# Kernel tuning notes

Hardware: AMD Instinct MI355X
Metric: run time of the kernel (lower is better)

Reference implementation:

```python
import jax, jax.numpy as jnp
import numpy as np


def pw_dist_sq(X, Y):
    xx = jnp.sum(X * X, axis=1)[:, None]   # [N,1]
    yy = jnp.sum(Y * Y, axis=1)[None, :]   # [1,N]
    xy = X @ Y.T                            # [N,N]
    return jnp.maximum(xx + yy - 2.0 * xy, 0.0)


def setup_inputs() -> dict:
    key = jax.random.key(0)
    k1, k2 = jax.random.split(key)
    N, D = 1024, 128
    X = jax.random.normal(k1, (N, D), dtype=jnp.float32)
    Y = jax.random.normal(k2, (N, D), dtype=jnp.float32)
    return {"X": X, "Y": Y, "h": 1}


def reference(X, Y, h):
    h = float(h)
    inv_h2 = 1.0 / (h * h)
    sq_dists = pw_dist_sq(X, Y)                       # [N,N]
    K = jnp.exp(-0.5 * inv_h2 * sq_dists)             # [N,N]
    # d_K[i,j,:] = -(X[i]-Y[j])/h^2 * K[i,j]; returned reduced over j
    diff = X[:, None, :] - Y[None, :, :]              # [N,N,D]
    d_K_sum = jnp.sum(-diff * inv_h2 * K[:, :, None], axis=1)  # [N,D]
    return K, d_K_sum
```

## Files before the change

kernel.cpp:

```cpp
#include <hip/hip_runtime.h>

#define NN 1024
#define DD 128

typedef float f32x4 __attribute__((ext_vector_type(4)));
typedef _Float16 f16x4 __attribute__((ext_vector_type(4)));
typedef _Float16 f16x8 __attribute__((ext_vector_type(8)));

__device__ __forceinline__ f16x8 cvt8(f32x4 a, f32x4 b) {
  f16x8 r;
  r[0] = (_Float16)a.x; r[1] = (_Float16)a.y; r[2] = (_Float16)a.z; r[3] = (_Float16)a.w;
  r[4] = (_Float16)b.x; r[5] = (_Float16)b.y; r[6] = (_Float16)b.z; r[7] = (_Float16)b.w;
  return r;
}

__device__ __forceinline__ void bar_lds() {
  asm volatile("s_waitcnt lgkmcnt(0)" ::: "memory");
  __builtin_amdgcn_s_barrier();
  asm volatile("" ::: "memory");
}

#define WS_PART 8192

__global__ __launch_bounds__(256, 2) void gk_main(const float* __restrict__ X,
                                                  const float* __restrict__ Y,
                                                  const int* __restrict__ hp,
                                                  float* __restrict__ out,
                                                  float* __restrict__ ws) {
  __shared__ __align__(16) _Float16 Ks[16][136];
  __shared__ unsigned msc[16];
  __shared__ float Sred[16];

  const int tid  = threadIdx.x;
  const int js   = blockIdx.x;
  const int ib   = blockIdx.y;
  const int lane = tid & 63;
  const int w    = tid >> 6;
  const int g    = lane >> 4;
  const int li   = lane & 15;

  const float fh = (float)hp[0];
  const float inv_h2 = 1.0f / (fh * fh);

  const float* Xr = X + (size_t)(ib * 16 + li) * DD;
  f32x4 xa[4][2];
  #pragma unroll
  for (int kt = 0; kt < 4; ++kt) {
    int d0 = kt * 32 + g * 8;
    xa[kt][0] = *(const f32x4*)(Xr + d0);
    xa[kt][1] = *(const f32x4*)(Xr + d0 + 4);
  }
  const float* Yr0 = Y + (size_t)(js * 128 + w * 32 + li) * DD;
  const float* Yr1 = Yr0 + 16 * DD;
  f32x4 ya0[4][2], ya1[4][2];
  #pragma unroll
  for (int kt = 0; kt < 4; ++kt) {
    int d0 = kt * 32 + g * 8;
    ya0[kt][0] = *(const f32x4*)(Yr0 + d0);
    ya0[kt][1] = *(const f32x4*)(Yr0 + d0 + 4);
    ya1[kt][0] = *(const f32x4*)(Yr1 + d0);
    ya1[kt][1] = *(const f32x4*)(Yr1 + d0 + 4);
  }

  if (tid < 16) { msc[tid] = 0u; Sred[tid] = 0.0f; }
  bar_lds();

  float xx = 0.f;
  #pragma unroll
  for (int kt = 0; kt < 4; ++kt)
    #pragma unroll
    for (int c = 0; c < 4; ++c)
      xx += xa[kt][0][c] * xa[kt][0][c] + xa[kt][1][c] * xa[kt][1][c];
  xx += __shfl_xor(xx, 16); xx += __shfl_xor(xx, 32);

  f32x4 acc0 = {0.f, 0.f, 0.f, 0.f}, acc1 = {0.f, 0.f, 0.f, 0.f};
  float yy0 = 0.f, yy1 = 0.f;
  #pragma unroll
  for (int kt = 0; kt < 4; ++kt) {
    #pragma unroll
    for (int c = 0; c < 4; ++c) {
      yy0 += ya0[kt][0][c] * ya0[kt][0][c] + ya0[kt][1][c] * ya0[kt][1][c];
      yy1 += ya1[kt][0][c] * ya1[kt][0][c] + ya1[kt][1][c] * ya1[kt][1][c];
    }
    f16x8 bf = cvt8(xa[kt][0], xa[kt][1]);
    acc0 = __builtin_amdgcn_mfma_f32_16x16x32_f16(cvt8(ya0[kt][0], ya0[kt][1]), bf, acc0, 0, 0, 0);
    acc1 = __builtin_amdgcn_mfma_f32_16x16x32_f16(cvt8(ya1[kt][0], ya1[kt][1]), bf, acc1, 0, 0, 0);
  }

  const int dA = w * 32 + li;
  const int dB = dA + 16;
  float bpre0[4][8], bpre1[4][8];
  #pragma unroll
  for (int kt = 0; kt < 4; ++kt) {
    const float* Yb = Y + (size_t)(js * 128 + kt * 32 + g * 8) * DD;
    #pragma unroll
    for (int e = 0; e < 8; ++e) {
      bpre0[kt][e] = Yb[e * DD + dA];
      bpre1[kt][e] = Yb[e * DD + dB];
    }
  }

  yy0 += __shfl_xor(yy0, 16); yy0 += __shfl_xor(yy0, 32);
  yy1 += __shfl_xor(yy1, 16); yy1 += __shfl_xor(yy1, 32);

  float K[8];
  float m = 0.f, sp = 0.f;
  #pragma unroll
  for (int r = 0; r < 4; ++r) {
    float yj0 = __shfl(yy0, 4 * g + r);
    float yj1 = __shfl(yy1, 4 * g + r);
    float e0 = fminf((acc0[r] - 0.5f * (xx + yj0)) * inv_h2, 0.0f);
    float e1 = fminf((acc1[r] - 0.5f * (xx + yj1)) * inv_h2, 0.0f);
    K[r]     = exp2f(e0 * 1.44269504088896341f);
    K[4 + r] = exp2f(e1 * 1.44269504088896341f);
    m = fmaxf(m, fmaxf(K[r], K[4 + r]));
    sp += K[r] + K[4 + r];
  }
  {
    float* kb = out + (size_t)(ib * 16 + li) * NN + js * 128 + w * 32 + 4 * g;
    f32x4 k0 = { K[0], K[1], K[2], K[3] };
    f32x4 k1 = { K[4], K[5], K[6], K[7] };
    *(f32x4*)kb = k0;
    *(f32x4*)(kb + 16) = k1;
  }
  m = fmaxf(m, __shfl_xor(m, 16)); m = fmaxf(m, __shfl_xor(m, 32));
  sp += __shfl_xor(sp, 16);        sp += __shfl_xor(sp, 32);
  if (lane < 16) {
    atomicMax(&msc[li], __float_as_uint(m));
    atomicAdd(&Sred[li], sp);
  }
  bar_lds();

  if (tid < 16) ws[(size_t)js * NN + ib * 16 + tid] = Sred[tid];

  {
    unsigned ue = (msc[li] >> 23) & 0xffu;
    unsigned se = 266u - ue; if (se > 254u) se = 254u;
    float scale = __uint_as_float(se << 23);
    #pragma unroll
    for (int t = 0; t < 2; ++t) {
      f16x4 q;
      #pragma unroll
      for (int r = 0; r < 4; ++r) q[r] = (_Float16)(K[t * 4 + r] * scale);
      *(f16x4*)&Ks[li][w * 32 + t * 16 + 4 * g] = q;
    }
  }
  bar_lds();

  f32x4 c0 = {0.f, 0.f, 0.f, 0.f}, c1 = {0.f, 0.f, 0.f, 0.f};
  #pragma unroll
  for (int kt = 0; kt < 4; ++kt) {
    f16x8 af = *(const f16x8*)&Ks[li][kt * 32 + g * 8];
    f16x8 b0, b1;
    #pragma unroll
    for (int e = 0; e < 8; ++e) {
      b0[e] = (_Float16)bpre0[kt][e];
      b1[e] = (_Float16)bpre1[kt][e];
    }
    c0 = __builtin_amdgcn_mfma_f32_16x16x32_f16(af, b0, c0, 0, 0, 0);
    c1 = __builtin_amdgcn_mfma_f32_16x16x32_f16(af, b1, c1, 0, 0, 0);
  }

  float* pb = ws + WS_PART + (size_t)js * (NN * DD) + (size_t)(ib * 16) * DD;
  #pragma unroll
  for (int r = 0; r < 4; ++r) {
    int il = 4 * g + r;
    unsigned ue2 = (msc[il] >> 23) & 0xffu;
    unsigned se2 = 266u - ue2; if (se2 > 254u) se2 = 254u;
    float invs = __uint_as_float((254u - se2) << 23);
    pb[il * DD + dA] = c0[r] * invs;
    pb[il * DD + dB] = c1[r] * invs;
  }
}

__global__ __launch_bounds__(256) void dk_reduce(const float* __restrict__ X,
                                                 const int* __restrict__ hp,
                                                 const float* __restrict__ ws,
                                                 float* __restrict__ out) {
  const int unit = blockIdx.x * 256 + threadIdx.x;
  const int i  = unit >> 5;
  const int d0 = (unit & 31) * 4;
  const float fh = (float)hp[0];
  const float inv_h2 = 1.0f / (fh * fh);

  f32x4 acc = {0.f, 0.f, 0.f, 0.f};
  float s = 0.f;
  #pragma unroll
  for (int js = 0; js < 8; ++js) {
    f32x4 p = *(const f32x4*)(ws + WS_PART + (size_t)js * (NN * DD) + (size_t)i * DD + d0);
    acc.x += p.x; acc.y += p.y; acc.z += p.z; acc.w += p.w;
    s += ws[(size_t)js * NN + i];
  }
  f32x4 xv = *(const f32x4*)(X + (size_t)i * DD + d0);
  f32x4 r;
  r.x = (acc.x - s * xv.x) * inv_h2;
  r.y = (acc.y - s * xv.y) * inv_h2;
  r.z = (acc.z - s * xv.z) * inv_h2;
  r.w = (acc.w - s * xv.w) * inv_h2;
  *(f32x4*)(out + (size_t)NN * NN + (size_t)i * DD + d0) = r;
}

extern "C" void kernel_launch(void* const* d_in, const int* in_sizes, int n_in,
                              void* d_out, int out_size, void* d_ws, size_t ws_size,
                              hipStream_t stream) {
  const float* X  = (const float*)d_in[0];
  const float* Y  = (const float*)d_in[1];
  const int*   hp = (const int*)d_in[2];
  float* out = (float*)d_out;
  float* ws  = (float*)d_ws;

  hipLaunchKernelGGL(gk_main, dim3(8, 64), dim3(256), 0, stream, X, Y, hp, out, ws);
  hipLaunchKernelGGL(dk_reduce, dim3(128), dim3(256), 0, stream, X, hp, ws, out);
}
```

Measured before the change: 17.55 us.

## Fuse kernel and reduction into one block-per-row-tile kernel with online rescaling

```diff
diff --git a/kernel.cpp b/kernel.cpp
--- a/kernel.cpp
+++ b/kernel.cpp
@@ -4,8 +4,9 @@
 #define DD 128
 
 typedef float f32x4 __attribute__((ext_vector_type(4)));
-typedef _Float16 f16x4 __attribute__((ext_vector_type(4)));
 typedef _Float16 f16x8 __attribute__((ext_vector_type(8)));
+
+union H2 { unsigned u; _Float16 h[2]; };
 
 __device__ __forceinline__ f16x8 cvt8(f32x4 a, f32x4 b) {
   f16x8 r;
@@ -20,20 +21,15 @@
   asm volatile("" ::: "memory");
 }
 
-#define WS_PART 8192
-
-__global__ __launch_bounds__(256, 2) void gk_main(const float* __restrict__ X,
-                                                  const float* __restrict__ Y,
-                                                  const int* __restrict__ hp,
-                                                  float* __restrict__ out,
-                                                  float* __restrict__ ws) {
-  __shared__ __align__(16) _Float16 Ks[16][136];
-  __shared__ unsigned msc[16];
-  __shared__ float Sred[16];
+__global__ __launch_bounds__(512, 2) void gk_all(const float* __restrict__ X,
+                                                 const float* __restrict__ Y,
+                                                 const int* __restrict__ hp,
+                                                 float* __restrict__ out) {
+  __shared__ __align__(16) char smem[8][8192];
+  __shared__ float SredL[128];
 
   const int tid  = threadIdx.x;
-  const int js   = blockIdx.x;
-  const int ib   = blockIdx.y;
+  const int ib   = blockIdx.x;
   const int lane = tid & 63;
   const int w    = tid >> 6;
   const int g    = lane >> 4;
@@ -41,163 +37,170 @@
 
   const float fh = (float)hp[0];
   const float inv_h2 = 1.0f / (fh * fh);
+  const float L2E = 1.44269504088896341f;
+
+  unsigned* ytp = (unsigned*)smem[w];
 
   const float* Xr = X + (size_t)(ib * 16 + li) * DD;
-  f32x4 xa[4][2];
+  f16x8 xbf[4];
+  float xx = 0.f;
   #pragma unroll
   for (int kt = 0; kt < 4; ++kt) {
     int d0 = kt * 32 + g * 8;
-    xa[kt][0] = *(const f32x4*)(Xr + d0);
-    xa[kt][1] = *(const f32x4*)(Xr + d0 + 4);
-  }
-  const float* Yr0 = Y + (size_t)(js * 128 + w * 32 + li) * DD;
-  const float* Yr1 = Yr0 + 16 * DD;
-  f32x4 ya0[4][2], ya1[4][2];
+    f32x4 a = *(const f32x4*)(Xr + d0);
+    f32x4 b = *(const f32x4*)(Xr + d0 + 4);
+    #pragma unroll
+    for (int c = 0; c < 4; ++c) xx += a[c] * a[c] + b[c] * b[c];
+    xbf[kt] = cvt8(a, b);
+  }
+  xx += __shfl_xor(xx, 16); xx += __shfl_xor(xx, 32);
+
+  float M = 0.f;
+  unsigned se = 254u;
+  float sp = 0.f;
+  f32x4 c[8] = {};
+
+  f32x4 ya[16];
+  {
+    const float* Yr0 = Y + (size_t)(w * 32 + li) * DD;
+    const float* Yr1 = Yr0 + 16 * DD;
+    #pragma unroll
+    for (int kt = 0; kt < 4; ++kt) {
+      int d0 = kt * 32 + g * 8;
+      ya[kt * 4 + 0] = *(const f32x4*)(Yr0 + d0);
+      ya[kt * 4 + 1] = *(const f32x4*)(Yr0 + d0 + 4);
+      ya[kt * 4 + 2] = *(const f32x4*)(Yr1 + d0);
+      ya[kt * 4 + 3] = *(const f32x4*)(Yr1 + d0 + 4);
+    }
+  }
+
   #pragma unroll
-  for (int kt = 0; kt < 4; ++kt) {
-    int d0 = kt * 32 + g * 8;
-    ya0[kt][0] = *(const f32x4*)(Yr0 + d0);
-    ya0[kt][1] = *(const f32x4*)(Yr0 + d0 + 4);
-    ya1[kt][0] = *(const f32x4*)(Yr1 + d0);
-    ya1[kt][1] = *(const f32x4*)(Yr1 + d0 + 4);
-  }
-
-  if (tid < 16) { msc[tid] = 0u; Sred[tid] = 0.0f; }
+  for (int t = 0; t < 4; ++t) {
+    const int j0 = t * 256 + w * 32;
+
+    float yy0 = 0.f, yy1 = 0.f;
+    #pragma unroll
+    for (int kt = 0; kt < 4; ++kt)
+      #pragma unroll
+      for (int cc = 0; cc < 4; ++cc) {
+        yy0 += ya[kt * 4 + 0][cc] * ya[kt * 4 + 0][cc] + ya[kt * 4 + 1][cc] * ya[kt * 4 + 1][cc];
+        yy1 += ya[kt * 4 + 2][cc] * ya[kt * 4 + 2][cc] + ya[kt * 4 + 3][cc] * ya[kt * 4 + 3][cc];
+      }
+    f16x8 af0[4], af1[4];
+    #pragma unroll
+    for (int kt = 0; kt < 4; ++kt) {
+      af0[kt] = cvt8(ya[kt * 4 + 0], ya[kt * 4 + 1]);
+      af1[kt] = cvt8(ya[kt * 4 + 2], ya[kt * 4 + 3]);
+    }
+
+    if (t < 3) {
+      const float* Yr0 = Y + (size_t)((t + 1) * 256 + w * 32 + li) * DD;
+      const float* Yr1 = Yr0 + 16 * DD;
+      #pragma unroll
+      for (int kt = 0; kt < 4; ++kt) {
+        int d0 = kt * 32 + g * 8;
+        ya[kt * 4 + 0] = *(const f32x4*)(Yr0 + d0);
+        ya[kt * 4 + 1] = *(const f32x4*)(Yr0 + d0 + 4);
+        ya[kt * 4 + 2] = *(const f32x4*)(Yr1 + d0);
+        ya[kt * 4 + 3] = *(const f32x4*)(Yr1 + d0 + 4);
+      }
+    }
+
+    f32x4 acc0 = {0.f, 0.f, 0.f, 0.f}, acc1 = {0.f, 0.f, 0.f, 0.f};
+    #pragma unroll
+    for (int kt = 0; kt < 4; ++kt) {
+      int d0 = kt * 32 + g * 8;
+      #pragma unroll
+      for (int cc = 0; cc < 8; ++cc) {
+        H2 pk; pk.h[0] = af0[kt][cc]; pk.h[1] = af1[kt][cc];
+        ytp[(d0 + cc) * 16 + li] = pk.u;
+      }
+      acc0 = __builtin_amdgcn_mfma_f32_16x16x32_f16(af0[kt], xbf[kt], acc0, 0, 0, 0);
+      acc1 = __builtin_amdgcn_mfma_f32_16x16x32_f16(af1[kt], xbf[kt], acc1, 0, 0, 0);
+    }
+    yy0 += __shfl_xor(yy0, 16); yy0 += __shfl_xor(yy0, 32);
+    yy1 += __shfl_xor(yy1, 16); yy1 += __shfl_xor(yy1, 32);
+
+    float Kr[8];
+    float mt = 0.f;
+    #pragma unroll
+    for (int r = 0; r < 4; ++r) {
+      float yj0 = __shfl(yy0, 4 * g + r);
+      float yj1 = __shfl(yy1, 4 * g + r);
+      float e0 = fminf((acc0[r] - 0.5f * (xx + yj0)) * inv_h2, 0.0f);
+      float e1 = fminf((acc1[r] - 0.5f * (xx + yj1)) * inv_h2, 0.0f);
+      Kr[r]     = exp2f(e0 * L2E);
+      Kr[4 + r] = exp2f(e1 * L2E);
+      mt = fmaxf(mt, fmaxf(Kr[r], Kr[4 + r]));
+      sp += Kr[r] + Kr[4 + r];
+    }
+    {
+      float* kb = out + (size_t)(ib * 16 + li) * NN + j0 + 4 * g;
+      f32x4 k0 = { Kr[0], Kr[1], Kr[2], Kr[3] };
+      f32x4 k1 = { Kr[4], Kr[5], Kr[6], Kr[7] };
+      *(f32x4*)kb = k0;
+      *(f32x4*)(kb + 16) = k1;
+    }
+
+    mt = fmaxf(mt, __shfl_xor(mt, 16)); mt = fmaxf(mt, __shfl_xor(mt, 32));
+    float Mn = fmaxf(M, mt);
+    unsigned e8 = (__float_as_uint(Mn) >> 23) & 0xffu;
+    unsigned sen = 266u - e8; if (sen > 254u) sen = 254u;
+    float fac = __uint_as_float((127u + sen - se) << 23);
+    #pragma unroll
+    for (int dt = 0; dt < 8; ++dt) {
+      c[dt].x *= fac; c[dt].y *= fac; c[dt].z *= fac; c[dt].w *= fac;
+    }
+    M = Mn; se = sen;
+    float scale = __uint_as_float(se << 23);
+
+    f16x8 bq;
+    #pragma unroll
+    for (int r = 0; r < 4; ++r) {
+      bq[2 * r]     = (_Float16)(Kr[r] * scale);
+      bq[2 * r + 1] = (_Float16)(Kr[4 + r] * scale);
+    }
+
+    asm volatile("" ::: "memory");
+
+    #pragma unroll
+    for (int dt = 0; dt < 8; ++dt) {
+      f16x8 af = *(const f16x8*)((const char*)ytp + (dt * 16 + li) * 64 + g * 16);
+      c[dt] = __builtin_amdgcn_mfma_f32_16x16x32_f16(af, bq, c[dt], 0, 0, 0);
+    }
+    asm volatile("" ::: "memory");
+  }
+
+  sp += __shfl_xor(sp, 16); sp += __shfl_xor(sp, 32);
+  if (lane < 16) SredL[w * 16 + li] = sp;
+
+  float invs = __uint_as_float((254u - se) << 23);
+  float* pw = (float*)smem[w];
+  #pragma unroll
+  for (int dt = 0; dt < 8; ++dt) {
+    f32x4 v = { c[dt].x * invs, c[dt].y * invs, c[dt].z * invs, c[dt].w * invs };
+    *(f32x4*)(pw + li * 128 + dt * 16 + 4 * g) = v;
+  }
   bar_lds();
 
-  float xx = 0.f;
-  #pragma unroll
-  for (int kt = 0; kt < 4; ++kt)
-    #pragma unroll
-    for (int c = 0; c < 4; ++c)
-      xx += xa[kt][0][c] * xa[kt][0][c] + xa[kt][1][c] * xa[kt][1][c];
-  xx += __shfl_xor(xx, 16); xx += __shfl_xor(xx, 32);
-
-  f32x4 acc0 = {0.f, 0.f, 0.f, 0.f}, acc1 = {0.f, 0.f, 0.f, 0.f};
-  float yy0 = 0.f, yy1 = 0.f;
-  #pragma unroll
-  for (int kt = 0; kt < 4; ++kt) {
-    #pragma unroll
-    for (int c = 0; c < 4; ++c) {
-      yy0 += ya0[kt][0][c] * ya0[kt][0][c] + ya0[kt][1][c] * ya0[kt][1][c];
-      yy1 += ya1[kt][0][c] * ya1[kt][0][c] + ya1[kt][1][c] * ya1[kt][1][c];
-    }
-    f16x8 bf = cvt8(xa[kt][0], xa[kt][1]);
-    acc0 = __builtin_amdgcn_mfma_f32_16x16x32_f16(cvt8(ya0[kt][0], ya0[kt][1]), bf, acc0, 0, 0, 0);
-    acc1 = __builtin_amdgcn_mfma_f32_16x16x32_f16(cvt8(ya1[kt][0], ya1[kt][1]), bf, acc1, 0, 0, 0);
-  }
-
-  const int dA = w * 32 + li;
-  const int dB = dA + 16;
-  float bpre0[4][8], bpre1[4][8];
-  #pragma unroll
-  for (int kt = 0; kt < 4; ++kt) {
-    const float* Yb = Y + (size_t)(js * 128 + kt * 32 + g * 8) * DD;
-    #pragma unroll
-    for (int e = 0; e < 8; ++e) {
-      bpre0[kt][e] = Yb[e * DD + dA];
-      bpre1[kt][e] = Yb[e * DD + dB];
-    }
-  }
-
-  yy0 += __shfl_xor(yy0, 16); yy0 += __shfl_xor(yy0, 32);
-  yy1 += __shfl_xor(yy1, 16); yy1 += __shfl_xor(yy1, 32);
-
-  float K[8];
-  float m = 0.f, sp = 0.f;
-  #pragma unroll
-  for (int r = 0; r < 4; ++r) {
-    float yj0 = __shfl(yy0, 4 * g + r);
-    float yj1 = __shfl(yy1, 4 * g + r);
-    float e0 = fminf((acc0[r] - 0.5f * (xx + yj0)) * inv_h2, 0.0f);
-    float e1 = fminf((acc1[r] - 0.5f * (xx + yj1)) * inv_h2, 0.0f);
-    K[r]     = exp2f(e0 * 1.44269504088896341f);
-    K[4 + r] = exp2f(e1 * 1.44269504088896341f);
-    m = fmaxf(m, fmaxf(K[r], K[4 + r]));
-    sp += K[r] + K[4 + r];
-  }
   {
-    float* kb = out + (size_t)(ib * 16 + li) * NN + js * 128 + w * 32 + 4 * g;
-    f32x4 k0 = { K[0], K[1], K[2], K[3] };
-    f32x4 k1 = { K[4], K[5], K[6], K[7] };
-    *(f32x4*)kb = k0;
-    *(f32x4*)(kb + 16) = k1;
-  }
-  m = fmaxf(m, __shfl_xor(m, 16)); m = fmaxf(m, __shfl_xor(m, 32));
-  sp += __shfl_xor(sp, 16);        sp += __shfl_xor(sp, 32);
-  if (lane < 16) {
-    atomicMax(&msc[li], __float_as_uint(m));
-    atomicAdd(&Sred[li], sp);
-  }
-  bar_lds();
-
-  if (tid < 16) ws[(size_t)js * NN + ib * 16 + tid] = Sred[tid];
-
-  {
-    unsigned ue = (msc[li] >> 23) & 0xffu;
-    unsigned se = 266u - ue; if (se > 254u) se = 254u;
-    float scale = __uint_as_float(se << 23);
-    #pragma unroll
-    for (int t = 0; t < 2; ++t) {
-      f16x4 q;
-      #pragma unroll
-      for (int r = 0; r < 4; ++r) q[r] = (_Float16)(K[t * 4 + r] * scale);
-      *(f16x4*)&Ks[li][w * 32 + t * 16 + 4 * g] = q;
-    }
-  }
-  bar_lds();
-
-  f32x4 c0 = {0.f, 0.f, 0.f, 0.f}, c1 = {0.f, 0.f, 0.f, 0.f};
-  #pragma unroll
-  for (int kt = 0; kt < 4; ++kt) {
-    f16x8 af = *(const f16x8*)&Ks[li][kt * 32 + g * 8];
-    f16x8 b0, b1;
-    #pragma unroll
-    for (int e = 0; e < 8; ++e) {
-      b0[e] = (_Float16)bpre0[kt][e];
-      b1[e] = (_Float16)bpre1[kt][e];
-    }
-    c0 = __builtin_amdgcn_mfma_f32_16x16x32_f16(af, b0, c0, 0, 0, 0);
-    c1 = __builtin_amdgcn_mfma_f32_16x16x32_f16(af, b1, c1, 0, 0, 0);
-  }
-
-  float* pb = ws + WS_PART + (size_t)js * (NN * DD) + (size_t)(ib * 16) * DD;
-  #pragma unroll
-  for (int r = 0; r < 4; ++r) {
-    int il = 4 * g + r;
-    unsigned ue2 = (msc[il] >> 23) & 0xffu;
-    unsigned se2 = 266u - ue2; if (se2 > 254u) se2 = 254u;
-    float invs = __uint_as_float((254u - se2) << 23);
-    pb[il * DD + dA] = c0[r] * invs;
-    pb[il * DD + dB] = c1[r] * invs;
-  }
-}
-
-__global__ __launch_bounds__(256) void dk_reduce(const float* __restrict__ X,
-                                                 const int* __restrict__ hp,
-                                                 const float* __restrict__ ws,
-                                                 float* __restrict__ out) {
-  const int unit = blockIdx.x * 256 + threadIdx.x;
-  const int i  = unit >> 5;
-  const int d0 = (unit & 31) * 4;
-  const float fh = (float)hp[0];
-  const float inv_h2 = 1.0f / (fh * fh);
-
-  f32x4 acc = {0.f, 0.f, 0.f, 0.f};
-  float s = 0.f;
-  #pragma unroll
-  for (int js = 0; js < 8; ++js) {
-    f32x4 p = *(const f32x4*)(ws + WS_PART + (size_t)js * (NN * DD) + (size_t)i * DD + d0);
-    acc.x += p.x; acc.y += p.y; acc.z += p.z; acc.w += p.w;
-    s += ws[(size_t)js * NN + i];
-  }
-  f32x4 xv = *(const f32x4*)(X + (size_t)i * DD + d0);
-  f32x4 r;
-  r.x = (acc.x - s * xv.x) * inv_h2;
-  r.y = (acc.y - s * xv.y) * inv_h2;
-  r.z = (acc.z - s * xv.z) * inv_h2;
-  r.w = (acc.w - s * xv.w) * inv_h2;
-  *(f32x4*)(out + (size_t)NN * NN + (size_t)i * DD + d0) = r;
+    int i = tid >> 5, dq = tid & 31;
+    f32x4 s = {0.f, 0.f, 0.f, 0.f};
+    float st = 0.f;
+    #pragma unroll
+    for (int w2 = 0; w2 < 8; ++w2) {
+      f32x4 p = *(const f32x4*)((const float*)smem[w2] + i * 128 + dq * 4);
+      s.x += p.x; s.y += p.y; s.z += p.z; s.w += p.w;
+      st += SredL[w2 * 16 + i];
+    }
+    f32x4 xv = *(const f32x4*)(X + (size_t)(ib * 16 + i) * DD + dq * 4);
+    f32x4 r;
+    r.x = (s.x - st * xv.x) * inv_h2;
+    r.y = (s.y - st * xv.y) * inv_h2;
+    r.z = (s.z - st * xv.z) * inv_h2;
+    r.w = (s.w - st * xv.w) * inv_h2;
+    *(f32x4*)(out + (size_t)NN * NN + (size_t)(ib * 16 + i) * DD + dq * 4) = r;
+  }
 }
 
 extern "C" void kernel_launch(void* const* d_in, const int* in_sizes, int n_in,
@@ -207,8 +210,6 @@
   const float* Y  = (const float*)d_in[1];
   const int*   hp = (const int*)d_in[2];
   float* out = (float*)d_out;
-  float* ws  = (float*)d_ws;
-
-  hipLaunchKernelGGL(gk_main, dim3(8, 64), dim3(256), 0, stream, X, Y, hp, out, ws);
-  hipLaunchKernelGGL(dk_reduce, dim3(128), dim3(256), 0, stream, X, hp, ws, out);
-}
+
+  hipLaunchKernelGGL(gk_all, dim3(64), dim3(512), 0, stream, X, Y, hp, out);
+}
```

Result: slower. 25.05 us (+42.8%).
